# Kernel optimization log

Hardware: AMD Instinct MI355X
Metric: run time of the kernel (lower is better)

Reference implementation:

```python
import jax, jax.numpy as jnp
import numpy as np

B, NX, C, KX = 16, 8192, 128, 16  # batch, grid size, channels, retained positive modes


def setup_inputs() -> dict:
    key = jax.random.key(0)
    k1, k2, k3 = jax.random.split(key, 3)
    x = jax.random.normal(k1, (B, NX, C), dtype=jnp.float32)
    scale = 1.0 / (C ** 2)
    w_real = scale * jax.random.uniform(k2, (KX + 1, C, C), dtype=jnp.float32)
    w_imag = scale * jax.random.uniform(k3, (KX + 1, C, C), dtype=jnp.float32)
    return {"x": x, "w_real": w_real, "w_imag": w_imag}


def reference(x, w_real, w_imag):
    # x: (b, nx, c); weights: (kx+1, c, c) complex
    nx = x.shape[1]
    k1 = w_real.shape[0]  # kx + 1 retained frequencies
    w = w_real + 1j * w_imag
    fx = jnp.fft.rfft(x, axis=-2)  # (b, nx//2+1, c) complex
    # torch.matmul(weights, fx[:, :kx+1, :, None])[..., 0]:
    # out[b,k,i] = sum_j w[k,i,j] * fx[b,k,j]
    out_ft = jnp.einsum('kij,bkj->bki', w, fx[:, :k1, :])
    # zero-pad truncated spectrum back to full rfft length, then inverse
    pad = nx // 2 + 1 - k1
    out_full = jnp.pad(out_ft, ((0, 0), (0, pad), (0, 0)))
    return jnp.fft.irfft(out_full, n=nx, axis=-2)
```

## Files before the change

kernel.cpp:

```cpp
#include <hip/hip_runtime.h>
#include <math.h>

#define B_     16
#define NX_    8192
#define C_     128
#define K1_    17
#define QW_    20
#define NC_    64
#define NH_    4096

typedef float v2f __attribute__((ext_vector_type(2)));
typedef float v4f __attribute__((ext_vector_type(4)));

#define GPART_F  ((size_t)B_ * K1_ * 2 * NC_ * C_)
#define ACOEF_F  ((size_t)B_ * K1_ * C_ * 2)
#define TRIG_OFF (GPART_F + ACOEF_F)


__global__ __launch_bounds__(256) void k_fwd(const float* __restrict__ x,
                                             float* __restrict__ ws) {
    __shared__ v4f smem[2 * 64 * 19];

    float* gpart = ws;
    const int b = blockIdx.y;
    const int c = blockIdx.x;
    const int t = threadIdx.x;
    const int jq  = t & 31;
    const int sub = (t >> 5) & 1;
    const int w   = t >> 6;
    const int i0  = c * 64;

    {
        float2* tg  = (float2*)smem;
        float2* tgg = (float2*)(ws + TRIG_OFF) + (size_t)c * (64 * QW_);
        for (int idx = t; idx < 64 * QW_; idx += 256) {
            int i = idx / QW_;
            int q = idx - i * QW_;
            float2 v = make_float2(0.f, 0.f);
            int k = (q < 9) ? (2 * q) : ((q >= 10 && q < 18) ? (2 * (q - 10) + 1) : -1);
            if (k >= 0) {
                int m = (k * (i0 + i)) & (NX_ - 1);
                float rev = (float)m * (1.0f / (float)NX_);
                v = make_float2(__builtin_amdgcn_cosf(rev),
                                __builtin_amdgcn_sinf(rev));
            }
            tg[idx] = v;
            if (b == 0) tgg[idx] = v;
        }
    }
    __syncthreads();

    v4f gr[9], gs[9];
#pragma unroll
    for (int kk = 0; kk < 9; ++kk) { gr[kk] = (v4f)(0.f); gs[kk] = (v4f)(0.f); }

    const size_t xb = (size_t)b * NX_ * C_;
    const int ibase = w * 16;
    const float sg = sub ? -1.f : 1.f;
    const float* tp = (const float*)smem + ((size_t)ibase * QW_ + sub * 10) * 2;
    const float* xlo_p = x + xb + (size_t)(i0 + ibase) * C_ + 4 * jq;
    const float* xhi_p = xlo_p + (size_t)NH_ * C_;

#pragma unroll 4
    for (int s = 0; s < 16; ++s) {
        v4f xlo = *(const v4f*)(xlo_p + (size_t)s * C_);
        v4f xhi = *(const v4f*)(xhi_p + (size_t)s * C_);
        v4f xs = __builtin_elementwise_fma(xhi, (v4f)(sg), xlo);
        const float* tr = tp + (size_t)s * (2 * QW_);
        float4 t0 = *(const float4*)(tr + 0);
        float4 t1 = *(const float4*)(tr + 4);
        float4 t2 = *(const float4*)(tr + 8);
        float4 t3 = *(const float4*)(tr + 12);
        float2 t4 = *(const float2*)(tr + 16);
        gr[0] = __builtin_elementwise_fma(xs, (v4f)(t0.x), gr[0]);
        gs[0] = __builtin_elementwise_fma(xs, (v4f)(t0.y), gs[0]);
        gr[1] = __builtin_elementwise_fma(xs, (v4f)(t0.z), gr[1]);
        gs[1] = __builtin_elementwise_fma(xs, (v4f)(t0.w), gs[1]);
        gr[2] = __builtin_elementwise_fma(xs, (v4f)(t1.x), gr[2]);
        gs[2] = __builtin_elementwise_fma(xs, (v4f)(t1.y), gs[2]);
        gr[3] = __builtin_elementwise_fma(xs, (v4f)(t1.z), gr[3]);
        gs[3] = __builtin_elementwise_fma(xs, (v4f)(t1.w), gs[3]);
        gr[4] = __builtin_elementwise_fma(xs, (v4f)(t2.x), gr[4]);
        gs[4] = __builtin_elementwise_fma(xs, (v4f)(t2.y), gs[4]);
        gr[5] = __builtin_elementwise_fma(xs, (v4f)(t2.z), gr[5]);
        gs[5] = __builtin_elementwise_fma(xs, (v4f)(t2.w), gs[5]);
        gr[6] = __builtin_elementwise_fma(xs, (v4f)(t3.x), gr[6]);
        gs[6] = __builtin_elementwise_fma(xs, (v4f)(t3.y), gs[6]);
        gr[7] = __builtin_elementwise_fma(xs, (v4f)(t3.z), gr[7]);
        gs[7] = __builtin_elementwise_fma(xs, (v4f)(t3.w), gs[7]);
        gr[8] = __builtin_elementwise_fma(xs, (v4f)(t4.x), gr[8]);
        gs[8] = __builtin_elementwise_fma(xs, (v4f)(t4.y), gs[8]);
    }

    const int lid = t & 63;
    __syncthreads();
    if (w >= 2) {
        v4f* p = smem + ((size_t)(w - 2) * 64 + lid) * 19;
#pragma unroll
        for (int kk = 0; kk < 9; ++kk) { p[2 * kk] = gr[kk]; p[2 * kk + 1] = gs[kk]; }
    }
    __syncthreads();
    if (w < 2) {
        const v4f* p = smem + ((size_t)w * 64 + lid) * 19;
#pragma unroll
        for (int kk = 0; kk < 9; ++kk) { gr[kk] += p[2 * kk]; gs[kk] += p[2 * kk + 1]; }
    }
    __syncthreads();
    if (w == 1) {
        v4f* p = smem + (size_t)lid * 19;
#pragma unroll
        for (int kk = 0; kk < 9; ++kk) { p[2 * kk] = gr[kk]; p[2 * kk + 1] = gs[kk]; }
    }
    __syncthreads();
    if (w == 0) {
        const v4f* p = smem + (size_t)lid * 19;
#pragma unroll
        for (int kk = 0; kk < 9; ++kk) {
            gr[kk] += p[2 * kk];
            gs[kk] += p[2 * kk + 1];
            if (sub == 0 || kk < 8) {
                int k = sub ? 2 * kk + 1 : 2 * kk;
                float* gpR = gpart + ((((size_t)b * K1_ + k) * 2 + 0) * NC_ + c) * C_ + 4 * jq;
                float* gpS = gpart + ((((size_t)b * K1_ + k) * 2 + 1) * NC_ + c) * C_ + 4 * jq;
                *(v4f*)gpR = gr[kk];
                *(v4f*)gpS = gs[kk];
            }
        }
    }
}

__global__ __launch_bounds__(1024) void k_mix(const float* __restrict__ wr_g,
                                              const float* __restrict__ wi_g,
                                              float* __restrict__ ws) {
    const int k = blockIdx.x;
    const int b = blockIdx.y;
    const int t = threadIdx.x;

    const float* gpart = ws;
    float2* acoef = (float2*)(ws + GPART_F);

    __shared__ float part[8][C_];
    __shared__ float gsum[2][C_];
    __shared__ float hp[16][C_];

    {
        const int ch = t & 127, ri = (t >> 7) & 1, sh = t >> 8;
        const float* base = gpart
            + (((size_t)b * K1_ + k) * 2 + ri) * ((size_t)NC_ * C_) + ch;
        float g = 0.f;
#pragma unroll
        for (int s = 0; s < 16; ++s) g += base[(size_t)(sh * 16 + s) * C_];
        part[sh * 2 + ri][ch] = g;
    }
    __syncthreads();
    if (t < 256) {
        const int ch = t & 127, ri = t >> 7;
        gsum[ri][ch] = part[ri][ch] + part[2 + ri][ch]
                     + part[4 + ri][ch] + part[6 + ri][ch];
    }
    __syncthreads();

    {
        const int i = t & 127, q = t >> 7;
        float hr = 0.f, hi = 0.f;
        const float* wrp = wr_g + ((size_t)k * C_ + i) * C_;
        const float* wip = wi_g + ((size_t)k * C_ + i) * C_;
#pragma unroll
        for (int jjj = 0; jjj < 16; ++jjj) {
            int jj = q * 16 + jjj;
            float wr = wrp[jj], wi = wip[jj];
            float a = gsum[0][jj], cc = gsum[1][jj];
            hr = fmaf(wr, a, hr); hr = fmaf( wi, cc, hr);
            hi = fmaf(wi, a, hi); hi = fmaf(-wr, cc, hi);
        }
        hp[q * 2 + 0][i] = hr;
        hp[q * 2 + 1][i] = hi;
    }
    __syncthreads();
    if (t < 128) {
        const int i = t;
        float hr = 0.f, hi = 0.f;
#pragma unroll
        for (int q = 0; q < 8; ++q) { hr += hp[q * 2][i]; hi += hp[q * 2 + 1][i]; }
        float cf = (k == 0 ? 1.0f : 2.0f) / (float)NX_;
        acoef[((size_t)b * K1_ + k) * C_ + i] = make_float2(cf * hr, -cf * hi);
    }
}

__global__ __launch_bounds__(256) void k_inv(float* __restrict__ out,
                                             const float* __restrict__ ws) {
    const float4* acoef4 = (const float4*)(ws + GPART_F);
    const float* trigg = ws + TRIG_OFF;
    const int b = blockIdx.y;
    const int c = blockIdx.x;
    const int t = threadIdx.x;
    const int jp = t & 63;
    const int h = __builtin_amdgcn_readfirstlane(t >> 6);
    const int i0 = c * 64;

    v2f arE[9], aiE[9], arO[8], aiO[8];
#pragma unroll
    for (int q = 0; q < 9; ++q) {
        float4 a = acoef4[((size_t)b * K1_ + 2 * q) * (C_ / 2) + jp];
        arE[q] = (v2f){a.x, a.z}; aiE[q] = (v2f){a.y, a.w};
    }
#pragma unroll
    for (int q = 0; q < 8; ++q) {
        float4 a = acoef4[((size_t)b * K1_ + 2 * q + 1) * (C_ / 2) + jp];
        arO[q] = (v2f){a.x, a.z}; aiO[q] = (v2f){a.y, a.w};
    }

    const float* trow = trigg + ((size_t)c * 64 + h * 16) * (2 * QW_);
    const size_t ob = (size_t)b * NX_ * C_;
    float* olo = out + ob + (size_t)(i0 + h * 16) * C_ + 2 * jp;
    float* ohi = olo + (size_t)NH_ * C_;

#pragma unroll 4
    for (int s = 0; s < 16; ++s) {
        const float* tr = trow + (size_t)s * (2 * QW_);
        float4 e0 = *(const float4*)(tr + 0);
        float4 e1 = *(const float4*)(tr + 4);
        float4 e2 = *(const float4*)(tr + 8);
        float4 e3 = *(const float4*)(tr + 12);
        float2 e4 = *(const float2*)(tr + 16);
        float4 o0 = *(const float4*)(tr + 20);
        float4 o1 = *(const float4*)(tr + 24);
        float4 o2 = *(const float4*)(tr + 28);
        float4 o3 = *(const float4*)(tr + 32);
        v2f Se = (v2f)(0.f), So = (v2f)(0.f);
        Se = __builtin_elementwise_fma(arE[0], (v2f)(e0.x), Se);
        Se = __builtin_elementwise_fma(aiE[0], (v2f)(e0.y), Se);
        Se = __builtin_elementwise_fma(arE[1], (v2f)(e0.z), Se);
        Se = __builtin_elementwise_fma(aiE[1], (v2f)(e0.w), Se);
        Se = __builtin_elementwise_fma(arE[2], (v2f)(e1.x), Se);
        Se = __builtin_elementwise_fma(aiE[2], (v2f)(e1.y), Se);
        Se = __builtin_elementwise_fma(arE[3], (v2f)(e1.z), Se);
        Se = __builtin_elementwise_fma(aiE[3], (v2f)(e1.w), Se);
        Se = __builtin_elementwise_fma(arE[4], (v2f)(e2.x), Se);
        Se = __builtin_elementwise_fma(aiE[4], (v2f)(e2.y), Se);
        Se = __builtin_elementwise_fma(arE[5], (v2f)(e2.z), Se);
        Se = __builtin_elementwise_fma(aiE[5], (v2f)(e2.w), Se);
        Se = __builtin_elementwise_fma(arE[6], (v2f)(e3.x), Se);
        Se = __builtin_elementwise_fma(aiE[6], (v2f)(e3.y), Se);
        Se = __builtin_elementwise_fma(arE[7], (v2f)(e3.z), Se);
        Se = __builtin_elementwise_fma(aiE[7], (v2f)(e3.w), Se);
        Se = __builtin_elementwise_fma(arE[8], (v2f)(e4.x), Se);
        Se = __builtin_elementwise_fma(aiE[8], (v2f)(e4.y), Se);
        So = __builtin_elementwise_fma(arO[0], (v2f)(o0.x), So);
        So = __builtin_elementwise_fma(aiO[0], (v2f)(o0.y), So);
        So = __builtin_elementwise_fma(arO[1], (v2f)(o0.z), So);
        So = __builtin_elementwise_fma(aiO[1], (v2f)(o0.w), So);
        So = __builtin_elementwise_fma(arO[2], (v2f)(o1.x), So);
        So = __builtin_elementwise_fma(aiO[2], (v2f)(o1.y), So);
        So = __builtin_elementwise_fma(arO[3], (v2f)(o1.z), So);
        So = __builtin_elementwise_fma(aiO[3], (v2f)(o1.w), So);
        So = __builtin_elementwise_fma(arO[4], (v2f)(o2.x), So);
        So = __builtin_elementwise_fma(aiO[4], (v2f)(o2.y), So);
        So = __builtin_elementwise_fma(arO[5], (v2f)(o2.z), So);
        So = __builtin_elementwise_fma(aiO[5], (v2f)(o2.w), So);
        So = __builtin_elementwise_fma(arO[6], (v2f)(o3.x), So);
        So = __builtin_elementwise_fma(aiO[6], (v2f)(o3.y), So);
        So = __builtin_elementwise_fma(arO[7], (v2f)(o3.z), So);
        So = __builtin_elementwise_fma(aiO[7], (v2f)(o3.w), So);
        *(v2f*)(olo + (size_t)s * C_) = Se + So;
        *(v2f*)(ohi + (size_t)s * C_) = Se - So;
    }
}

extern "C" void kernel_launch(void* const* d_in, const int* in_sizes, int n_in,
                              void* d_out, int out_size, void* d_ws, size_t ws_size,
                              hipStream_t stream) {
    const float* x  = (const float*)d_in[0];
    const float* wr = (const float*)d_in[1];
    const float* wi = (const float*)d_in[2];
    float* out = (float*)d_out;
    float* ws  = (float*)d_ws;

    k_fwd<<<dim3(NC_, B_), 256, 0, stream>>>(x, ws);
    k_mix<<<dim3(K1_, B_), 1024, 0, stream>>>(wr, wi, ws);
    k_inv<<<dim3(NC_, B_), 256, 0, stream>>>(out, ws);
}
```

Baseline: 51.62 us.

## Fuse three stages into persistent kernel with software grid barriers

Replaces the three kernel launches (forward projection, spectral mix, inverse) with one persistent kernel whose grid is sized from occupancy queries, separated by atomic-based grid barriers. It aims to remove the inter-kernel launch gaps and tail effects. The mix stage now uses 256-thread blocks instead of 1024. It adds a memset plus host-side device-property and occupancy queries on every call, and it relies on all blocks being co-resident. The old three-kernel path is kept as a fallback.

```diff
diff --git a/kernel.cpp b/kernel.cpp
--- a/kernel.cpp
+++ b/kernel.cpp
@@ -15,52 +15,310 @@
 #define GPART_F  ((size_t)B_ * K1_ * 2 * NC_ * C_)
 #define ACOEF_F  ((size_t)B_ * K1_ * C_ * 2)
 #define TRIG_OFF (GPART_F + ACOEF_F)
-
-
-__global__ __launch_bounds__(256) void k_fwd(const float* __restrict__ x,
-                                             float* __restrict__ ws) {
+#define TRIG_F   ((size_t)NC_ * 64 * 2 * QW_)
+#define BAR_OFF  (TRIG_OFF + TRIG_F)
+
+__device__ __forceinline__ void grid_barrier(unsigned* bar, unsigned nblk,
+                                             unsigned target) {
+    __syncthreads();
+    if (threadIdx.x == 0) {
+        __threadfence();
+        unsigned prev = atomicAdd(bar, 1u);
+        if (prev + 1 == nblk) {
+            atomicExch(bar, 0u);
+            __threadfence();
+            atomicExch(bar + 1, target);
+        } else {
+            while (__hip_atomic_load(bar + 1, __ATOMIC_RELAXED,
+                                     __HIP_MEMORY_SCOPE_AGENT) < target)
+                __builtin_amdgcn_s_sleep(2);
+        }
+        __threadfence();
+    }
+    __syncthreads();
+}
+
+__global__ __launch_bounds__(256, 4) void k_all(
+        const float* __restrict__ x,
+        const float* __restrict__ wr_g,
+        const float* __restrict__ wi_g,
+        float* __restrict__ out,
+        float* __restrict__ ws,
+        unsigned* __restrict__ bar) {
     __shared__ v4f smem[2 * 64 * 19];
 
     float* gpart = ws;
-    const int b = blockIdx.y;
-    const int c = blockIdx.x;
+    float2* acoef = (float2*)(ws + GPART_F);
+    const int nblk = gridDim.x;
     const int t = threadIdx.x;
     const int jq  = t & 31;
     const int sub = (t >> 5) & 1;
     const int w   = t >> 6;
-    const int i0  = c * 64;
-
+
+    for (int tile = blockIdx.x; tile < B_ * NC_; tile += nblk) {
+        const int b = tile >> 6;
+        const int c = tile & 63;
+        const int i0 = c * 64;
+
+        {
+            float2* tg  = (float2*)smem;
+            float2* tgg = (float2*)(ws + TRIG_OFF) + (size_t)c * (64 * QW_);
+            for (int idx = t; idx < 64 * QW_; idx += 256) {
+                int i = idx / QW_;
+                int q = idx - i * QW_;
+                float2 v = make_float2(0.f, 0.f);
+                int k = (q < 9) ? (2 * q) : ((q >= 10 && q < 18) ? (2 * (q - 10) + 1) : -1);
+                if (k >= 0) {
+                    int m = (k * (i0 + i)) & (NX_ - 1);
+                    float rev = (float)m * (1.0f / (float)NX_);
+                    v = make_float2(__builtin_amdgcn_cosf(rev),
+                                    __builtin_amdgcn_sinf(rev));
+                }
+                tg[idx] = v;
+                if (b == 0) tgg[idx] = v;
+            }
+        }
+        __syncthreads();
+
+        v4f gr[9], gs[9];
+#pragma unroll
+        for (int kk = 0; kk < 9; ++kk) { gr[kk] = (v4f)(0.f); gs[kk] = (v4f)(0.f); }
+
+        const size_t xb = (size_t)b * NX_ * C_;
+        const int ibase = w * 16;
+        const float sg = sub ? -1.f : 1.f;
+        const float* tp = (const float*)smem + ((size_t)ibase * QW_ + sub * 10) * 2;
+        const float* xlo_p = x + xb + (size_t)(i0 + ibase) * C_ + 4 * jq;
+        const float* xhi_p = xlo_p + (size_t)NH_ * C_;
+
+#pragma unroll 4
+        for (int s = 0; s < 16; ++s) {
+            v4f xlo = *(const v4f*)(xlo_p + (size_t)s * C_);
+            v4f xhi = *(const v4f*)(xhi_p + (size_t)s * C_);
+            v4f xs = __builtin_elementwise_fma(xhi, (v4f)(sg), xlo);
+            const float* tr = tp + (size_t)s * (2 * QW_);
+            float4 t0 = *(const float4*)(tr + 0);
+            float4 t1 = *(const float4*)(tr + 4);
+            float4 t2 = *(const float4*)(tr + 8);
+            float4 t3 = *(const float4*)(tr + 12);
+            float2 t4 = *(const float2*)(tr + 16);
+            gr[0] = __builtin_elementwise_fma(xs, (v4f)(t0.x), gr[0]);
+            gs[0] = __builtin_elementwise_fma(xs, (v4f)(t0.y), gs[0]);
+            gr[1] = __builtin_elementwise_fma(xs, (v4f)(t0.z), gr[1]);
+            gs[1] = __builtin_elementwise_fma(xs, (v4f)(t0.w), gs[1]);
+            gr[2] = __builtin_elementwise_fma(xs, (v4f)(t1.x), gr[2]);
+            gs[2] = __builtin_elementwise_fma(xs, (v4f)(t1.y), gs[2]);
+            gr[3] = __builtin_elementwise_fma(xs, (v4f)(t1.z), gr[3]);
+            gs[3] = __builtin_elementwise_fma(xs, (v4f)(t1.w), gs[3]);
+            gr[4] = __builtin_elementwise_fma(xs, (v4f)(t2.x), gr[4]);
+            gs[4] = __builtin_elementwise_fma(xs, (v4f)(t2.y), gs[4]);
+            gr[5] = __builtin_elementwise_fma(xs, (v4f)(t2.z), gr[5]);
+            gs[5] = __builtin_elementwise_fma(xs, (v4f)(t2.w), gs[5]);
+            gr[6] = __builtin_elementwise_fma(xs, (v4f)(t3.x), gr[6]);
+            gs[6] = __builtin_elementwise_fma(xs, (v4f)(t3.y), gs[6]);
+            gr[7] = __builtin_elementwise_fma(xs, (v4f)(t3.z), gr[7]);
+            gs[7] = __builtin_elementwise_fma(xs, (v4f)(t3.w), gs[7]);
+            gr[8] = __builtin_elementwise_fma(xs, (v4f)(t4.x), gr[8]);
+            gs[8] = __builtin_elementwise_fma(xs, (v4f)(t4.y), gs[8]);
+        }
+
+        const int lid = t & 63;
+        __syncthreads();
+        if (w >= 2) {
+            v4f* p = smem + ((size_t)(w - 2) * 64 + lid) * 19;
+#pragma unroll
+            for (int kk = 0; kk < 9; ++kk) { p[2 * kk] = gr[kk]; p[2 * kk + 1] = gs[kk]; }
+        }
+        __syncthreads();
+        if (w < 2) {
+            const v4f* p = smem + ((size_t)w * 64 + lid) * 19;
+#pragma unroll
+            for (int kk = 0; kk < 9; ++kk) { gr[kk] += p[2 * kk]; gs[kk] += p[2 * kk + 1]; }
+        }
+        __syncthreads();
+        if (w == 1) {
+            v4f* p = smem + (size_t)lid * 19;
+#pragma unroll
+            for (int kk = 0; kk < 9; ++kk) { p[2 * kk] = gr[kk]; p[2 * kk + 1] = gs[kk]; }
+        }
+        __syncthreads();
+        if (w == 0) {
+            const v4f* p = smem + (size_t)lid * 19;
+#pragma unroll
+            for (int kk = 0; kk < 9; ++kk) {
+                gr[kk] += p[2 * kk];
+                gs[kk] += p[2 * kk + 1];
+                if (sub == 0 || kk < 8) {
+                    int k = sub ? 2 * kk + 1 : 2 * kk;
+                    float* gpR = gpart + ((((size_t)b * K1_ + k) * 2 + 0) * NC_ + c) * C_ + 4 * jq;
+                    float* gpS = gpart + ((((size_t)b * K1_ + k) * 2 + 1) * NC_ + c) * C_ + 4 * jq;
+                    *(v4f*)gpR = gr[kk];
+                    *(v4f*)gpS = gs[kk];
+                }
+            }
+        }
+        __syncthreads();
+    }
+
+    grid_barrier(bar, (unsigned)nblk, 1u);
+
+    for (int job = blockIdx.x; job < B_ * K1_; job += nblk) {
+        const int k  = job % K1_;
+        const int bb = job / K1_;
+        const int i = t & 127;
+        const int h = t >> 7;
+        float* grs = (float*)smem;
+        float* gss = grs + C_;
+        float* trr = gss + C_;
+        float* tii = trr + C_;
+
+        const float* baseR = gpart + (((size_t)bb * K1_ + k) * 2 + 0) * ((size_t)NC_ * C_);
+        const float* baseS = gpart + (((size_t)bb * K1_ + k) * 2 + 1) * ((size_t)NC_ * C_);
+        float gr = 0.f, gs = 0.f;
+#pragma unroll
+        for (int s = 0; s < 32; ++s) {
+            gr += baseR[(size_t)(h * 32 + s) * C_ + i];
+            gs += baseS[(size_t)(h * 32 + s) * C_ + i];
+        }
+        if (h) { trr[i] = gr; tii[i] = gs; }
+        __syncthreads();
+        if (!h) { grs[i] = gr + trr[i]; gss[i] = gs + tii[i]; }
+        __syncthreads();
+
+        float hr = 0.f, hi = 0.f;
+        const float* wrp = wr_g + ((size_t)k * C_ + i) * C_;
+        const float* wip = wi_g + ((size_t)k * C_ + i) * C_;
+#pragma unroll 8
+        for (int jj = h * 64; jj < h * 64 + 64; ++jj) {
+            float wr = wrp[jj], wi = wip[jj];
+            float a = grs[jj], cc = gss[jj];
+            hr = fmaf(wr, a, hr); hr = fmaf( wi, cc, hr);
+            hi = fmaf(wi, a, hi); hi = fmaf(-wr, cc, hi);
+        }
+        __syncthreads();
+        if (h) { trr[i] = hr; tii[i] = hi; }
+        __syncthreads();
+        if (!h) {
+            hr += trr[i]; hi += tii[i];
+            float cf = (k == 0 ? 1.0f : 2.0f) / (float)NX_;
+            acoef[((size_t)bb * K1_ + k) * C_ + i] = make_float2(cf * hr, -cf * hi);
+        }
+        __syncthreads();
+    }
+
+    grid_barrier(bar, (unsigned)nblk, 2u);
+
+    for (int tile = blockIdx.x; tile < B_ * NC_; tile += nblk) {
+        const int b = tile >> 6;
+        const int c = tile & 63;
+        const int i0 = c * 64;
+        const float4* acoef4 = (const float4*)(ws + GPART_F);
+        const float* trigg = ws + TRIG_OFF;
+        const int jp = t & 63;
+        const int h = __builtin_amdgcn_readfirstlane(t >> 6);
+
+        v2f arE[9], aiE[9], arO[8], aiO[8];
+#pragma unroll
+        for (int q = 0; q < 9; ++q) {
+            float4 a = acoef4[((size_t)b * K1_ + 2 * q) * (C_ / 2) + jp];
+            arE[q] = (v2f){a.x, a.z}; aiE[q] = (v2f){a.y, a.w};
+        }
+#pragma unroll
+        for (int q = 0; q < 8; ++q) {
+            float4 a = acoef4[((size_t)b * K1_ + 2 * q + 1) * (C_ / 2) + jp];
+            arO[q] = (v2f){a.x, a.z}; aiO[q] = (v2f){a.y, a.w};
+        }
+
+        const float* trow = trigg + ((size_t)c * 64 + h * 16) * (2 * QW_);
+        const size_t ob = (size_t)b * NX_ * C_;
+        float* olo = out + ob + (size_t)(i0 + h * 16) * C_ + 2 * jp;
+        float* ohi = olo + (size_t)NH_ * C_;
+
+#pragma unroll 4
+        for (int s = 0; s < 16; ++s) {
+            const float* tr = trow + (size_t)s * (2 * QW_);
+            float4 e0 = *(const float4*)(tr + 0);
+            float4 e1 = *(const float4*)(tr + 4);
+            float4 e2 = *(const float4*)(tr + 8);
+            float4 e3 = *(const float4*)(tr + 12);
+            float2 e4 = *(const float2*)(tr + 16);
+            float4 o0 = *(const float4*)(tr + 20);
+            float4 o1 = *(const float4*)(tr + 24);
+            float4 o2 = *(const float4*)(tr + 28);
+            float4 o3 = *(const float4*)(tr + 32);
+            v2f Se = (v2f)(0.f), So = (v2f)(0.f);
+            Se = __builtin_elementwise_fma(arE[0], (v2f)(e0.x), Se);
+            Se = __builtin_elementwise_fma(aiE[0], (v2f)(e0.y), Se);
+            Se = __builtin_elementwise_fma(arE[1], (v2f)(e0.z), Se);
+            Se = __builtin_elementwise_fma(aiE[1], (v2f)(e0.w), Se);
+            Se = __builtin_elementwise_fma(arE[2], (v2f)(e1.x), Se);
+            Se = __builtin_elementwise_fma(aiE[2], (v2f)(e1.y), Se);
+            Se = __builtin_elementwise_fma(arE[3], (v2f)(e1.z), Se);
+            Se = __builtin_elementwise_fma(aiE[3], (v2f)(e1.w), Se);
+            Se = __builtin_elementwise_fma(arE[4], (v2f)(e2.x), Se);
+            Se = __builtin_elementwise_fma(aiE[4], (v2f)(e2.y), Se);
+            Se = __builtin_elementwise_fma(arE[5], (v2f)(e2.z), Se);
+            Se = __builtin_elementwise_fma(aiE[5], (v2f)(e2.w), Se);
+            Se = __builtin_elementwise_fma(arE[6], (v2f)(e3.x), Se);
+            Se = __builtin_elementwise_fma(aiE[6], (v2f)(e3.y), Se);
+            Se = __builtin_elementwise_fma(arE[7], (v2f)(e3.z), Se);
+            Se = __builtin_elementwise_fma(aiE[7], (v2f)(e3.w), Se);
+            Se = __builtin_elementwise_fma(arE[8], (v2f)(e4.x), Se);
+            Se = __builtin_elementwise_fma(aiE[8], (v2f)(e4.y), Se);
+            So = __builtin_elementwise_fma(arO[0], (v2f)(o0.x), So);
+            So = __builtin_elementwise_fma(aiO[0], (v2f)(o0.y), So);
+            So = __builtin_elementwise_fma(arO[1], (v2f)(o0.z), So);
+            So = __builtin_elementwise_fma(aiO[1], (v2f)(o0.w), So);
+            So = __builtin_elementwise_fma(arO[2], (v2f)(o1.x), So);
+            So = __builtin_elementwise_fma(aiO[2], (v2f)(o1.y), So);
+            So = __builtin_elementwise_fma(arO[3], (v2f)(o1.z), So);
+            So = __builtin_elementwise_fma(aiO[3], (v2f)(o1.w), So);
+            So = __builtin_elementwise_fma(arO[4], (v2f)(o2.x), So);
+            So = __builtin_elementwise_fma(aiO[4], (v2f)(o2.y), So);
+            So = __builtin_elementwise_fma(arO[5], (v2f)(o2.z), So);
+            So = __builtin_elementwise_fma(aiO[5], (v2f)(o2.w), So);
+            So = __builtin_elementwise_fma(arO[6], (v2f)(o3.x), So);
+            So = __builtin_elementwise_fma(aiO[6], (v2f)(o3.y), So);
+            So = __builtin_elementwise_fma(arO[7], (v2f)(o3.z), So);
+            So = __builtin_elementwise_fma(aiO[7], (v2f)(o3.w), So);
+            *(v2f*)(olo + (size_t)s * C_) = Se + So;
+            *(v2f*)(ohi + (size_t)s * C_) = Se - So;
+        }
+    }
+}
+
+__global__ __launch_bounds__(256) void k_fwd(const float* __restrict__ x,
+                                             float* __restrict__ ws) {
+    __shared__ v4f smem[2 * 64 * 19];
+    float* gpart = ws;
+    const int b = blockIdx.y, c = blockIdx.x, t = threadIdx.x;
+    const int jq = t & 31, sub = (t >> 5) & 1, w = t >> 6, i0 = c * 64;
     {
         float2* tg  = (float2*)smem;
         float2* tgg = (float2*)(ws + TRIG_OFF) + (size_t)c * (64 * QW_);
         for (int idx = t; idx < 64 * QW_; idx += 256) {
-            int i = idx / QW_;
-            int q = idx - i * QW_;
+            int i = idx / QW_, q = idx - i * QW_;
             float2 v = make_float2(0.f, 0.f);
             int k = (q < 9) ? (2 * q) : ((q >= 10 && q < 18) ? (2 * (q - 10) + 1) : -1);
             if (k >= 0) {
                 int m = (k * (i0 + i)) & (NX_ - 1);
                 float rev = (float)m * (1.0f / (float)NX_);
-                v = make_float2(__builtin_amdgcn_cosf(rev),
-                                __builtin_amdgcn_sinf(rev));
+                v = make_float2(__builtin_amdgcn_cosf(rev), __builtin_amdgcn_sinf(rev));
             }
             tg[idx] = v;
             if (b == 0) tgg[idx] = v;
         }
     }
     __syncthreads();
-
     v4f gr[9], gs[9];
 #pragma unroll
     for (int kk = 0; kk < 9; ++kk) { gr[kk] = (v4f)(0.f); gs[kk] = (v4f)(0.f); }
-
     const size_t xb = (size_t)b * NX_ * C_;
     const int ibase = w * 16;
     const float sg = sub ? -1.f : 1.f;
     const float* tp = (const float*)smem + ((size_t)ibase * QW_ + sub * 10) * 2;
     const float* xlo_p = x + xb + (size_t)(i0 + ibase) * C_ + 4 * jq;
     const float* xhi_p = xlo_p + (size_t)NH_ * C_;
-
 #pragma unroll 4
     for (int s = 0; s < 16; ++s) {
         v4f xlo = *(const v4f*)(xlo_p + (size_t)s * C_);
@@ -91,7 +349,6 @@
         gr[8] = __builtin_elementwise_fma(xs, (v4f)(t4.x), gr[8]);
         gs[8] = __builtin_elementwise_fma(xs, (v4f)(t4.y), gs[8]);
     }
-
     const int lid = t & 63;
     __syncthreads();
     if (w >= 2) {
@@ -132,21 +389,15 @@
 __global__ __launch_bounds__(1024) void k_mix(const float* __restrict__ wr_g,
                                               const float* __restrict__ wi_g,
                                               float* __restrict__ ws) {
-    const int k = blockIdx.x;
-    const int b = blockIdx.y;
-    const int t = threadIdx.x;
-
+    const int k = blockIdx.x, b = blockIdx.y, t = threadIdx.x;
     const float* gpart = ws;
     float2* acoef = (float2*)(ws + GPART_F);
-
     __shared__ float part[8][C_];
     __shared__ float gsum[2][C_];
     __shared__ float hp[16][C_];
-
     {
         const int ch = t & 127, ri = (t >> 7) & 1, sh = t >> 8;
-        const float* base = gpart
-            + (((size_t)b * K1_ + k) * 2 + ri) * ((size_t)NC_ * C_) + ch;
+        const float* base = gpart + (((size_t)b * K1_ + k) * 2 + ri) * ((size_t)NC_ * C_) + ch;
         float g = 0.f;
 #pragma unroll
         for (int s = 0; s < 16; ++s) g += base[(size_t)(sh * 16 + s) * C_];
@@ -155,11 +406,9 @@
     __syncthreads();
     if (t < 256) {
         const int ch = t & 127, ri = t >> 7;
-        gsum[ri][ch] = part[ri][ch] + part[2 + ri][ch]
-                     + part[4 + ri][ch] + part[6 + ri][ch];
-    }
-    __syncthreads();
-
+        gsum[ri][ch] = part[ri][ch] + part[2 + ri][ch] + part[4 + ri][ch] + part[6 + ri][ch];
+    }
+    __syncthreads();
     {
         const int i = t & 127, q = t >> 7;
         float hr = 0.f, hi = 0.f;
@@ -191,13 +440,10 @@
                                              const float* __restrict__ ws) {
     const float4* acoef4 = (const float4*)(ws + GPART_F);
     const float* trigg = ws + TRIG_OFF;
-    const int b = blockIdx.y;
-    const int c = blockIdx.x;
-    const int t = threadIdx.x;
+    const int b = blockIdx.y, c = blockIdx.x, t = threadIdx.x;
     const int jp = t & 63;
     const int h = __builtin_amdgcn_readfirstlane(t >> 6);
     const int i0 = c * 64;
-
     v2f arE[9], aiE[9], arO[8], aiO[8];
 #pragma unroll
     for (int q = 0; q < 9; ++q) {
@@ -209,12 +455,10 @@
         float4 a = acoef4[((size_t)b * K1_ + 2 * q + 1) * (C_ / 2) + jp];
         arO[q] = (v2f){a.x, a.z}; aiO[q] = (v2f){a.y, a.w};
     }
-
     const float* trow = trigg + ((size_t)c * 64 + h * 16) * (2 * QW_);
     const size_t ob = (size_t)b * NX_ * C_;
     float* olo = out + ob + (size_t)(i0 + h * 16) * C_ + 2 * jp;
     float* ohi = olo + (size_t)NH_ * C_;
-
 #pragma unroll 4
     for (int s = 0; s < 16; ++s) {
         const float* tr = trow + (size_t)s * (2 * QW_);
@@ -275,8 +519,26 @@
     const float* wi = (const float*)d_in[2];
     float* out = (float*)d_out;
     float* ws  = (float*)d_ws;
-
-    k_fwd<<<dim3(NC_, B_), 256, 0, stream>>>(x, ws);
-    k_mix<<<dim3(K1_, B_), 1024, 0, stream>>>(wr, wi, ws);
-    k_inv<<<dim3(NC_, B_), 256, 0, stream>>>(out, ws);
+    unsigned* bar = (unsigned*)(ws + BAR_OFF);
+
+    int dev = 0;
+    (void)hipGetDevice(&dev);
+    hipDeviceProp_t prop;
+    hipError_t e1 = hipGetDeviceProperties(&prop, dev);
+    int perCU = 0;
+    hipError_t e2 = hipOccupancyMaxActiveBlocksPerMultiprocessor(
+        &perCU, (const void*)k_all, 256, 0);
+
+    int grid = (e1 == hipSuccess && e2 == hipSuccess && perCU > 0)
+                   ? perCU * prop.multiProcessorCount : 0;
+    if (grid > B_ * NC_) grid = B_ * NC_;
+
+    if (grid >= 256) {
+        hipMemsetAsync(bar, 0, 2 * sizeof(unsigned), stream);
+        k_all<<<grid, 256, 0, stream>>>(x, wr, wi, out, ws, bar);
+    } else {
+        k_fwd<<<dim3(NC_, B_), 256, 0, stream>>>(x, ws);
+        k_mix<<<dim3(K1_, B_), 1024, 0, stream>>>(wr, wi, ws);
+        k_inv<<<dim3(NC_, B_), 256, 0, stream>>>(out, ws);
+    }
 }
```

New measurement: 191.3 us. 271% more time.

## Split forward and inverse kernels across more blocks to raise occupancy

Applied to the files above, without the earlier changes.

The forward DFT kernel now splits channels into two halves per block. Each thread handles 4 channels and a quarter of the frequency columns, so it holds 5 accumulator pairs instead of 9, and the shared reduction buffer shrinks. The inverse kernel processes 32 grid rows per block instead of 64, which doubles its grid. Both changes aim to increase parallelism and occupancy on the many-CU GPU. The cost is redundant trig-table generation in the forward pass and more per-block overhead, since the frequency coefficients are reloaded twice as often in the inverse pass.

```diff
diff --git a/kernel.cpp b/kernel.cpp
--- a/kernel.cpp
+++ b/kernel.cpp
@@ -7,6 +7,7 @@
 #define K1_    17
 #define QW_    20
 #define NC_    64
+#define NCI_   128
 #define NH_    4096
 
 typedef float v2f __attribute__((ext_vector_type(2)));
@@ -19,16 +20,17 @@
 
 __global__ __launch_bounds__(256) void k_fwd(const float* __restrict__ x,
                                              float* __restrict__ ws) {
-    __shared__ v4f smem[2 * 64 * 19];
+    __shared__ v4f smem[2 * 64 * 11];
 
     float* gpart = ws;
-    const int b = blockIdx.y;
-    const int c = blockIdx.x;
+    const int b     = blockIdx.y;
+    const int c     = blockIdx.x >> 1;
+    const int chalf = blockIdx.x & 1;
     const int t = threadIdx.x;
-    const int jq  = t & 31;
-    const int sub = (t >> 5) & 1;
-    const int w   = t >> 6;
-    const int i0  = c * 64;
+    const int jq = t & 15;
+    const int su = (t >> 4) & 3;
+    const int w  = t >> 6;
+    const int i0 = c * 64;
 
     {
         float2* tg  = (float2*)smem;
@@ -45,20 +47,20 @@
                                 __builtin_amdgcn_sinf(rev));
             }
             tg[idx] = v;
-            if (b == 0) tgg[idx] = v;
+            if (b == 0 && chalf == 0) tgg[idx] = v;
         }
     }
     __syncthreads();
 
-    v4f gr[9], gs[9];
-#pragma unroll
-    for (int kk = 0; kk < 9; ++kk) { gr[kk] = (v4f)(0.f); gs[kk] = (v4f)(0.f); }
+    v4f gr[5], gs[5];
+#pragma unroll
+    for (int kk = 0; kk < 5; ++kk) { gr[kk] = (v4f)(0.f); gs[kk] = (v4f)(0.f); }
 
     const size_t xb = (size_t)b * NX_ * C_;
     const int ibase = w * 16;
-    const float sg = sub ? -1.f : 1.f;
-    const float* tp = (const float*)smem + ((size_t)ibase * QW_ + sub * 10) * 2;
-    const float* xlo_p = x + xb + (size_t)(i0 + ibase) * C_ + 4 * jq;
+    const float sg = (su < 2) ? 1.f : -1.f;
+    const float* tp = (const float*)smem + (size_t)ibase * (2 * QW_) + su * 10;
+    const float* xlo_p = x + xb + (size_t)(i0 + ibase) * C_ + chalf * 64 + 4 * jq;
     const float* xhi_p = xlo_p + (size_t)NH_ * C_;
 
 #pragma unroll 4
@@ -67,61 +69,54 @@
         v4f xhi = *(const v4f*)(xhi_p + (size_t)s * C_);
         v4f xs = __builtin_elementwise_fma(xhi, (v4f)(sg), xlo);
         const float* tr = tp + (size_t)s * (2 * QW_);
-        float4 t0 = *(const float4*)(tr + 0);
-        float4 t1 = *(const float4*)(tr + 4);
-        float4 t2 = *(const float4*)(tr + 8);
-        float4 t3 = *(const float4*)(tr + 12);
-        float2 t4 = *(const float2*)(tr + 16);
-        gr[0] = __builtin_elementwise_fma(xs, (v4f)(t0.x), gr[0]);
-        gs[0] = __builtin_elementwise_fma(xs, (v4f)(t0.y), gs[0]);
-        gr[1] = __builtin_elementwise_fma(xs, (v4f)(t0.z), gr[1]);
-        gs[1] = __builtin_elementwise_fma(xs, (v4f)(t0.w), gs[1]);
-        gr[2] = __builtin_elementwise_fma(xs, (v4f)(t1.x), gr[2]);
-        gs[2] = __builtin_elementwise_fma(xs, (v4f)(t1.y), gs[2]);
-        gr[3] = __builtin_elementwise_fma(xs, (v4f)(t1.z), gr[3]);
-        gs[3] = __builtin_elementwise_fma(xs, (v4f)(t1.w), gs[3]);
-        gr[4] = __builtin_elementwise_fma(xs, (v4f)(t2.x), gr[4]);
-        gs[4] = __builtin_elementwise_fma(xs, (v4f)(t2.y), gs[4]);
-        gr[5] = __builtin_elementwise_fma(xs, (v4f)(t2.z), gr[5]);
-        gs[5] = __builtin_elementwise_fma(xs, (v4f)(t2.w), gs[5]);
-        gr[6] = __builtin_elementwise_fma(xs, (v4f)(t3.x), gr[6]);
-        gs[6] = __builtin_elementwise_fma(xs, (v4f)(t3.y), gs[6]);
-        gr[7] = __builtin_elementwise_fma(xs, (v4f)(t3.z), gr[7]);
-        gs[7] = __builtin_elementwise_fma(xs, (v4f)(t3.w), gs[7]);
-        gr[8] = __builtin_elementwise_fma(xs, (v4f)(t4.x), gr[8]);
-        gs[8] = __builtin_elementwise_fma(xs, (v4f)(t4.y), gs[8]);
+        float4 a0 = *(const float4*)(tr + 0);
+        float4 a1 = *(const float4*)(tr + 4);
+        float2 a2 = *(const float2*)(tr + 8);
+        gr[0] = __builtin_elementwise_fma(xs, (v4f)(a0.x), gr[0]);
+        gs[0] = __builtin_elementwise_fma(xs, (v4f)(a0.y), gs[0]);
+        gr[1] = __builtin_elementwise_fma(xs, (v4f)(a0.z), gr[1]);
+        gs[1] = __builtin_elementwise_fma(xs, (v4f)(a0.w), gs[1]);
+        gr[2] = __builtin_elementwise_fma(xs, (v4f)(a1.x), gr[2]);
+        gs[2] = __builtin_elementwise_fma(xs, (v4f)(a1.y), gs[2]);
+        gr[3] = __builtin_elementwise_fma(xs, (v4f)(a1.z), gr[3]);
+        gs[3] = __builtin_elementwise_fma(xs, (v4f)(a1.w), gs[3]);
+        gr[4] = __builtin_elementwise_fma(xs, (v4f)(a2.x), gr[4]);
+        gs[4] = __builtin_elementwise_fma(xs, (v4f)(a2.y), gs[4]);
     }
 
     const int lid = t & 63;
     __syncthreads();
     if (w >= 2) {
-        v4f* p = smem + ((size_t)(w - 2) * 64 + lid) * 19;
-#pragma unroll
-        for (int kk = 0; kk < 9; ++kk) { p[2 * kk] = gr[kk]; p[2 * kk + 1] = gs[kk]; }
+        v4f* p = smem + ((size_t)(w - 2) * 64 + lid) * 11;
+#pragma unroll
+        for (int kk = 0; kk < 5; ++kk) { p[2 * kk] = gr[kk]; p[2 * kk + 1] = gs[kk]; }
     }
     __syncthreads();
     if (w < 2) {
-        const v4f* p = smem + ((size_t)w * 64 + lid) * 19;
-#pragma unroll
-        for (int kk = 0; kk < 9; ++kk) { gr[kk] += p[2 * kk]; gs[kk] += p[2 * kk + 1]; }
+        const v4f* p = smem + ((size_t)w * 64 + lid) * 11;
+#pragma unroll
+        for (int kk = 0; kk < 5; ++kk) { gr[kk] += p[2 * kk]; gs[kk] += p[2 * kk + 1]; }
     }
     __syncthreads();
     if (w == 1) {
-        v4f* p = smem + (size_t)lid * 19;
-#pragma unroll
-        for (int kk = 0; kk < 9; ++kk) { p[2 * kk] = gr[kk]; p[2 * kk + 1] = gs[kk]; }
+        v4f* p = smem + (size_t)lid * 11;
+#pragma unroll
+        for (int kk = 0; kk < 5; ++kk) { p[2 * kk] = gr[kk]; p[2 * kk + 1] = gs[kk]; }
     }
     __syncthreads();
     if (w == 0) {
-        const v4f* p = smem + (size_t)lid * 19;
-#pragma unroll
-        for (int kk = 0; kk < 9; ++kk) {
+        const v4f* p = smem + (size_t)lid * 11;
+#pragma unroll
+        for (int kk = 0; kk < 5; ++kk) {
             gr[kk] += p[2 * kk];
             gs[kk] += p[2 * kk + 1];
-            if (sub == 0 || kk < 8) {
-                int k = sub ? 2 * kk + 1 : 2 * kk;
-                float* gpR = gpart + ((((size_t)b * K1_ + k) * 2 + 0) * NC_ + c) * C_ + 4 * jq;
-                float* gpS = gpart + ((((size_t)b * K1_ + k) * 2 + 1) * NC_ + c) * C_ + 4 * jq;
+            int q = su * 5 + kk;
+            int k = (q < 9) ? (2 * q) : ((q >= 10 && q < 18) ? (2 * (q - 10) + 1) : -1);
+            if (k >= 0) {
+                float* gpR = gpart + ((((size_t)b * K1_ + k) * 2 + 0) * NC_ + c) * C_
+                           + chalf * 64 + 4 * jq;
+                float* gpS = gpart + ((((size_t)b * K1_ + k) * 2 + 1) * NC_ + c) * C_
+                           + chalf * 64 + 4 * jq;
                 *(v4f*)gpR = gr[kk];
                 *(v4f*)gpS = gs[kk];
             }
@@ -132,21 +127,15 @@
 __global__ __launch_bounds__(1024) void k_mix(const float* __restrict__ wr_g,
                                               const float* __restrict__ wi_g,
                                               float* __restrict__ ws) {
-    const int k = blockIdx.x;
-    const int b = blockIdx.y;
-    const int t = threadIdx.x;
-
+    const int k = blockIdx.x, b = blockIdx.y, t = threadIdx.x;
     const float* gpart = ws;
     float2* acoef = (float2*)(ws + GPART_F);
-
     __shared__ float part[8][C_];
     __shared__ float gsum[2][C_];
     __shared__ float hp[16][C_];
-
     {
         const int ch = t & 127, ri = (t >> 7) & 1, sh = t >> 8;
-        const float* base = gpart
-            + (((size_t)b * K1_ + k) * 2 + ri) * ((size_t)NC_ * C_) + ch;
+        const float* base = gpart + (((size_t)b * K1_ + k) * 2 + ri) * ((size_t)NC_ * C_) + ch;
         float g = 0.f;
 #pragma unroll
         for (int s = 0; s < 16; ++s) g += base[(size_t)(sh * 16 + s) * C_];
@@ -155,11 +144,9 @@
     __syncthreads();
     if (t < 256) {
         const int ch = t & 127, ri = t >> 7;
-        gsum[ri][ch] = part[ri][ch] + part[2 + ri][ch]
-                     + part[4 + ri][ch] + part[6 + ri][ch];
-    }
-    __syncthreads();
-
+        gsum[ri][ch] = part[ri][ch] + part[2 + ri][ch] + part[4 + ri][ch] + part[6 + ri][ch];
+    }
+    __syncthreads();
     {
         const int i = t & 127, q = t >> 7;
         float hr = 0.f, hi = 0.f;
@@ -191,12 +178,10 @@
                                              const float* __restrict__ ws) {
     const float4* acoef4 = (const float4*)(ws + GPART_F);
     const float* trigg = ws + TRIG_OFF;
-    const int b = blockIdx.y;
-    const int c = blockIdx.x;
-    const int t = threadIdx.x;
+    const int b = blockIdx.y, c2 = blockIdx.x, t = threadIdx.x;
     const int jp = t & 63;
     const int h = __builtin_amdgcn_readfirstlane(t >> 6);
-    const int i0 = c * 64;
+    const int i0 = c2 * 32;
 
     v2f arE[9], aiE[9], arO[8], aiO[8];
 #pragma unroll
@@ -210,13 +195,13 @@
         arO[q] = (v2f){a.x, a.z}; aiO[q] = (v2f){a.y, a.w};
     }
 
-    const float* trow = trigg + ((size_t)c * 64 + h * 16) * (2 * QW_);
+    const float* trow = trigg + ((size_t)(i0 + h * 8)) * (2 * QW_);
     const size_t ob = (size_t)b * NX_ * C_;
-    float* olo = out + ob + (size_t)(i0 + h * 16) * C_ + 2 * jp;
+    float* olo = out + ob + (size_t)(i0 + h * 8) * C_ + 2 * jp;
     float* ohi = olo + (size_t)NH_ * C_;
 
 #pragma unroll 4
-    for (int s = 0; s < 16; ++s) {
+    for (int s = 0; s < 8; ++s) {
         const float* tr = trow + (size_t)s * (2 * QW_);
         float4 e0 = *(const float4*)(tr + 0);
         float4 e1 = *(const float4*)(tr + 4);
@@ -276,7 +261,7 @@
     float* out = (float*)d_out;
     float* ws  = (float*)d_ws;
 
-    k_fwd<<<dim3(NC_, B_), 256, 0, stream>>>(x, ws);
+    k_fwd<<<dim3(NC_ * 2, B_), 256, 0, stream>>>(x, ws);
     k_mix<<<dim3(K1_, B_), 1024, 0, stream>>>(wr, wi, ws);
-    k_inv<<<dim3(NC_, B_), 256, 0, stream>>>(out, ws);
-}
+    k_inv<<<dim3(NCI_, B_), 256, 0, stream>>>(out, ws);
+}
```

Measured after the change: 76.15 us. +47.5%, slower.
